# Kernel tuning notes

Hardware: AMD Instinct MI355X
Metric: run time of the kernel (lower is better)

Reference implementation:

```python
import jax, jax.numpy as jnp
import numpy as np

EMBED_DIM = 1024
NUM_HEADS = 16
HEAD_DIM = EMBED_DIM // NUM_HEADS


def setup_inputs() -> dict:
    key = jax.random.key(0)
    ks = jax.random.split(key, 9)
    B, S, D = 2, 2048, EMBED_DIM
    scale = 1.0 / np.sqrt(D)
    x = jax.random.normal(ks[0], (B, S, D), dtype=jnp.float32)
    # Linear params (torch nn.Linear: y = x @ W.T + b); store W as [out, in]
    Wq = jax.random.normal(ks[1], (D, D), dtype=jnp.float32) * scale
    bq = jnp.zeros((D,), dtype=jnp.float32)
    Wk = jax.random.normal(ks[2], (D, D), dtype=jnp.float32) * scale
    bk = jnp.zeros((D,), dtype=jnp.float32)
    Wv = jax.random.normal(ks[3], (D, D), dtype=jnp.float32) * scale
    bv = jnp.zeros((D,), dtype=jnp.float32)
    Wo = jax.random.normal(ks[4], (D, D), dtype=jnp.float32) * scale
    bo = jnp.zeros((D,), dtype=jnp.float32)
    return {"x": x, "Wq": Wq, "bq": bq, "Wk": Wk, "bk": bk,
            "Wv": Wv, "bv": bv, "Wo": Wo, "bo": bo}


def reference(x, Wq, bq, Wk, bk, Wv, bv, Wo, bo):
    B, S, D = x.shape
    H, Hd = NUM_HEADS, HEAD_DIM
    scaling = Hd ** -0.5
    # projections (torch Linear: x @ W.T + b)
    q = (x @ Wq.T + bq).reshape(B, S, H, Hd).transpose(0, 2, 1, 3)  # [B,H,S,Hd]
    k = (x @ Wk.T + bk).reshape(B, S, H, Hd).transpose(0, 2, 1, 3)
    v = (x @ Wv.T + bv).reshape(B, S, H, Hd).transpose(0, 2, 1, 3)
    # full score matrix, as in the original (no flash tiling)
    scores = jnp.einsum('bhqd,bhkd->bhqk', q, k) * scaling  # [B,H,S,S]
    attn = jax.nn.softmax(scores, axis=-1)
    # dropout is identity in eval mode
    out = jnp.einsum('bhqk,bhkd->bhqd', attn, v)  # [B,H,S,Hd]
    out = out.transpose(0, 2, 1, 3).reshape(B, S, D)
    return out @ Wo.T + bo
```

## Files before the change

### kernel.cpp

```cpp
#include <hip/hip_runtime.h>
#include <stdint.h>

typedef unsigned short u16;
typedef short short8 __attribute__((ext_vector_type(8)));
typedef float f32x4 __attribute__((ext_vector_type(4)));
typedef float f32x16 __attribute__((ext_vector_type(16)));
typedef float f32x2 __attribute__((ext_vector_type(2)));

__device__ __forceinline__ u16 f2bf_fast(float f) {
  union { float f; uint32_t u; } x;
  x.f = f;
  return (u16)((x.u + 0x8000u) >> 16);
}

__device__ __forceinline__ uint32_t pack2bf(float lo, float hi) {
  union { float f; uint32_t u; } a, b;
  a.f = lo; b.f = hi;
  return __builtin_amdgcn_perm(b.u + 0x8000u, a.u + 0x8000u, 0x07060302u);
}

__device__ __forceinline__ float bf2f(uint32_t u) {
  union { uint32_t u; float f; } x;
  x.u = u << 16;
  return x.f;
}

__device__ __forceinline__ uint32_t cvtpk(float lo, float hi) {
  uint32_t r;
  asm("v_cvt_pk_bf16_f32 %0, %1, %2" : "=v"(r) : "v"(lo), "v"(hi));
  return r;
}

__device__ __forceinline__ void permswap(uint32_t& a, uint32_t& b) {
  asm("v_permlane32_swap_b32 %0, %1" : "+v"(a), "+v"(b));
}

__device__ __forceinline__ void gload_lds16(const void* g, void* l) {
  __builtin_amdgcn_global_load_lds(
      (const __attribute__((address_space(1))) void*)g,
      (__attribute__((address_space(3))) void*)l, 16, 0, 0);
}

__device__ __forceinline__ f32x4 mfma16(short8 a, short8 b, f32x4 c) {
  return __builtin_amdgcn_mfma_f32_16x16x32_bf16(a, b, c, 0, 0, 0);
}

__device__ __forceinline__ f32x16 mfma32(short8 a, short8 b, f32x16 c) {
  return __builtin_amdgcn_mfma_f32_32x32x16_bf16(a, b, c, 0, 0, 0);
}

#define QSCALE 0.18033688011112042f

__global__ void pack_all(const float* __restrict__ x, const float* __restrict__ wq,
                         const float* __restrict__ wk, const float* __restrict__ wv,
                         const float* __restrict__ wo, u16* __restrict__ xp,
                         u16* __restrict__ wp) {
  const int gi = blockIdx.x * 256 + threadIdx.x;
  const int lane = gi & 63;
  const int kc = (gi >> 6) & 31;
  const int rt = gi >> 11;
  const int col = kc * 32 + (lane >> 4) * 8;
  const float* src;
  int row;
  if (rt < 256) {
    src = x;
    row = rt * 16 + (lane & 15);
  } else {
    const int wti = rt - 256;
    const int widx = wti >> 6;
    src = (widx == 0) ? wq : (widx == 1) ? wk : (widx == 2) ? wv : wo;
    row = (wti & 63) * 16 + (lane & 15);
  }
  const float4* p = (const float4*)(src + (size_t)row * 1024 + col);
  const float4 v0 = p[0], v1 = p[1];
  uint4 o;
  o.x = pack2bf(v0.x, v0.y);
  o.y = pack2bf(v0.z, v0.w);
  o.z = pack2bf(v1.x, v1.y);
  o.w = pack2bf(v1.z, v1.w);
  u16* dst = (rt < 256) ? xp : wp;
  const int og = (rt < 256) ? gi : gi - 524288;
  ((uint4*)dst)[og] = o;
}

__global__ __launch_bounds__(256, 3) void proj_qkv(
    const u16* __restrict__ xp, const u16* __restrict__ wp,
    const float* __restrict__ bq, const float* __restrict__ bk,
    const float* __restrict__ bv, u16* __restrict__ qw, u16* __restrict__ kw,
    u16* __restrict__ vw) {
  __shared__ __align__(16) u16 As[8192];
  __shared__ __align__(16) u16 Bs[8192];
  const int tid = threadIdx.x, lane = tid & 63, w = tid >> 6;
  const int quad = lane >> 4, l15 = lane & 15;

  const int bid = blockIdx.x;
  const int work = (bid & 7) * 96 + (bid >> 3);
  const bool isQK = work < 512;
  int at0, bt0, bm2, bn2;
  const u16 *Ap, *Bp;
  if (isQK) {
    bm2 = work >> 4; bn2 = work & 15;
    Ap = xp; at0 = bm2 * 8;
    Bp = wp; bt0 = bn2 * 8;
  } else {
    const int h = work - 512;
    bm2 = h >> 5; bn2 = h & 31;
    Ap = wp; at0 = 128 + bm2 * 8;
    Bp = xp; bt0 = bn2 * 8;
  }
  const int wr = w >> 1, wc = w & 1;
  const int bm = bm2 * 2 + wr, bn = bn2 * 2 + wc;

  auto stage = [&](int kc, int buf) {
#pragma unroll
    for (int i = 0; i < 4; ++i) {
      const int g = w * 4 + i;
      const int t = g & 7;
      const u16* src = (g < 8)
          ? (Ap + (((at0 + t) << 5) + kc) * 512 + lane * 8)
          : (Bp + (((bt0 + t) << 5) + kc) * 512 + lane * 8);
      u16* dst = ((g < 8) ? As : Bs) + (buf * 8 + t) * 512 + lane * 8;
      gload_lds16(src, dst);
    }
  };

  f32x4 acc[4][4] = {};

  stage(0, 0);
  __syncthreads();

  for (int kc = 0; kc < 32; ++kc) {
    const int cur = kc & 1;
    if (kc < 31) stage(kc + 1, cur ^ 1);

    const u16* Ab = As + cur * 4096;
    const u16* Bb = Bs + cur * 4096;
    short8 af[4], bf[4];
#pragma unroll
    for (int mt = 0; mt < 4; ++mt)
      af[mt] = *(const short8*)&Ab[((wr * 4 + mt) * 64 + lane) * 8];
#pragma unroll
    for (int nt = 0; nt < 4; ++nt)
      bf[nt] = *(const short8*)&Bb[((wc * 4 + nt) * 64 + lane) * 8];

#pragma unroll
    for (int mt = 0; mt < 4; ++mt)
#pragma unroll
      for (int nt = 0; nt < 4; ++nt)
        acc[mt][nt] = mfma16(af[mt], bf[nt], acc[mt][nt]);
    __syncthreads();
  }

#pragma unroll
  for (int nt = 0; nt < 4; ++nt) {
    const int n = bn * 64 + nt * 16 + l15;
#pragma unroll
    for (int mt = 0; mt < 4; ++mt)
#pragma unroll
      for (int r = 0; r < 4; ++r) {
        const int m = bm * 64 + mt * 16 + quad * 4 + r;
        const float a = acc[mt][nt][r];
        if (isQK) {
          const bool isQ = (bn < 16);
          const int nn = isQ ? n : n - 1024;
          const float v = isQ ? (a + bq[nn]) * QSCALE : a + bk[nn];
          u16* op = isQ ? qw : kw;
          const int b = m >> 11, s = m & 2047, hh = nn >> 6, d = nn & 63;
          op[((size_t)((b * 16 + hh) * 2048 + s)) * 64 + d] = f2bf_fast(v);
        } else {
          const float v = a + bv[m];
          const int b = n >> 11, s = n & 2047;
          vw[((size_t)(b * 1024 + m)) * 2048 + s] = f2bf_fast(v);
        }
      }
  }
}

__global__ __launch_bounds__(256, 4) void attn_kernel(
    const u16* __restrict__ Q, const u16* __restrict__ Kt,
    const u16* __restrict__ Vt, u16* __restrict__ awp) {
  __shared__ __align__(16) u16 Sm[16384];
  const int tid = threadIdx.x, lane = tid & 63, w = tid >> 6;
  const int l31 = lane & 31, hi = lane >> 5, l7 = lane & 7;
  const int qt = blockIdx.x;
  const int bh = blockIdx.y;

  const char* Qb = (const char*)(Q + ((size_t)bh * 2048 + qt * 128) * 64);
  const char* Kb = (const char*)(Kt + (size_t)bh * 2048 * 64);
  const char* Vb = (const char*)(Vt + (size_t)bh * 64 * 2048);

  auto stageKV = [&](int kt, int b) {
    u16* Kl = Sm + b * 4096;
    u16* Vl = Sm + 8192 + b * 4096;
#pragma unroll
    for (int i = 0; i < 2; ++i) {
      const int G = (w * 2 + i) * 64 + lane;
      const int r = G >> 3, sl = G & 7;
      gload_lds16(Kb + (size_t)(kt * 64 + r) * 128 + ((sl ^ (r & 7)) * 16),
                  &Kl[G * 8]);
      gload_lds16(Vb + (size_t)r * 4096 + kt * 128 + ((sl ^ (r & 7)) * 16),
                  &Vl[G * 8]);
    }
  };

#pragma unroll
  for (int i = 0; i < 4; ++i) {
    const int G = (w * 4 + i) * 64 + lane;
    const int row = G >> 3, sl = G & 7;
    u16* qdst = (G < 512) ? (Sm + 4096) : (Sm + 12288);
    gload_lds16(Qb + (size_t)row * 128 + ((sl ^ (row & 7)) * 16),
                &qdst[(G & 511) * 8]);
  }
  stageKV(0, 0);
  __syncthreads();

  const u16* qreg = (w < 2) ? (Sm + 4096) : (Sm + 12288);
  const int qr0 = (w & 1) * 32;
  short8 aq[4];
#pragma unroll
  for (int ds = 0; ds < 4; ++ds)
    aq[ds] = *(const short8*)&qreg[(qr0 + l31) * 64 + (((ds << 1) + hi) ^ l7) * 8];
  __syncthreads();

  f32x16 ot[2] = {};
  f32x2 l2 = {0.f, 0.f};

  for (int kt = 0; kt < 32; ++kt) {
    const int buf = kt & 1;
    if (kt < 31) stageKV(kt + 1, buf ^ 1);
    const u16* Kl = Sm + buf * 4096;
    const u16* Vl = Sm + 8192 + buf * 4096;

#pragma unroll
    for (int t = 0; t < 2; ++t) {
      f32x16 st = {};
      __builtin_amdgcn_s_setprio(1);
#pragma unroll
      for (int ds = 0; ds < 4; ++ds) {
        short8 kf = *(const short8*)&Kl[(t * 32 + l31) * 64 +
                                        (((ds << 1) + hi) ^ l7) * 8];
        st = mfma32(kf, aq[ds], st);
      }
      __builtin_amdgcn_s_setprio(0);
      float e[16];
#pragma unroll
      for (int i = 0; i < 16; ++i) e[i] = __builtin_amdgcn_exp2f(st[i]);
#pragma unroll
      for (int i = 0; i < 8; ++i) l2 += (f32x2){e[2 * i], e[2 * i + 1]};

      uint32_t p01 = cvtpk(e[0], e[1]),   p23 = cvtpk(e[2], e[3]);
      uint32_t p45 = cvtpk(e[4], e[5]),   p67 = cvtpk(e[6], e[7]);
      uint32_t p89 = cvtpk(e[8], e[9]),   pAB = cvtpk(e[10], e[11]);
      uint32_t pCD = cvtpk(e[12], e[13]), pEF = cvtpk(e[14], e[15]);
      permswap(p01, p45);
      permswap(p23, p67);
      permswap(p89, pCD);
      permswap(pAB, pEF);
      union { uint32_t u[4]; short8 s; } b0, b1;
      b0.u[0] = p01; b0.u[1] = p23; b0.u[2] = p45; b0.u[3] = p67;
      b1.u[0] = p89; b1.u[1] = pAB; b1.u[2] = pCD; b1.u[3] = pEF;

      __builtin_amdgcn_s_setprio(1);
#pragma unroll
      for (int dt = 0; dt < 2; ++dt) {
#pragma unroll
        for (int s2 = 0; s2 < 2; ++s2) {
          short8 vf = *(const short8*)&Vl[(dt * 32 + l31) * 64 +
                                          ((((t * 2 + s2) << 1) + hi) ^ l7) * 8];
          ot[dt] = mfma32(vf, s2 ? b1.s : b0.s, ot[dt]);
        }
      }
      __builtin_amdgcn_s_setprio(0);
    }
    if (kt < 31) __syncthreads();
  }

  const int b = bh >> 4, h = bh & 15;
  float l = l2.x + l2.y;
  l += __shfl_xor(l, 32);
  const float inv = __builtin_amdgcn_rcpf(l);
  const int rt = b * 128 + qt * 8 + w * 2 + (l31 >> 4);
#pragma unroll
  for (int dt = 0; dt < 2; ++dt) {
    const int kc = h * 2 + dt;
#pragma unroll
    for (int g = 0; g < 4; ++g) {
      const int ln = (lane & 15) + 16 * g;
      uint2 ov;
      ov.x = cvtpk(ot[dt][4 * g + 0] * inv, ot[dt][4 * g + 1] * inv);
      ov.y = cvtpk(ot[dt][4 * g + 2] * inv, ot[dt][4 * g + 3] * inv);
      *(uint2*)(awp + ((size_t)((rt * 32 + kc) * 64 + ln)) * 8 + hi * 4) = ov;
    }
  }
}

__global__ __launch_bounds__(512, 2) void out_proj(const u16* __restrict__ awp,
                                                   const u16* __restrict__ wp,
                                                   const float* __restrict__ bo,
                                                   float* __restrict__ out) {
  __shared__ __align__(16) u16 As[8192];
  __shared__ __align__(16) u16 Bs[8192];
  const int tid = threadIdx.x, lane = tid & 63, w = tid >> 6;
  const int quad = lane >> 4, l15 = lane & 15;

  const int bid = blockIdx.x;
  const int work = (bid & 7) * 32 + (bid >> 3);
  const int bm2 = work >> 3, bn2 = work & 7;
  const int at0 = bm2 * 8, bt0 = 192 + bn2 * 8;
  const int wr = w >> 2, wc = w & 3;

  auto stage = [&](int kc, int buf) {
#pragma unroll
    for (int i = 0; i < 2; ++i) {
      const int g = w * 2 + i;
      const int t = g & 7;
      const u16* src = (g < 8)
          ? (awp + (((at0 + t) << 5) + kc) * 512 + lane * 8)
          : (wp + (((bt0 + t) << 5) + kc) * 512 + lane * 8);
      u16* dst = ((g < 8) ? As : Bs) + (buf * 8 + t) * 512 + lane * 8;
      gload_lds16(src, dst);
    }
  };

  f32x4 acc[4][2] = {};

  stage(0, 0);
  __syncthreads();

  for (int kc = 0; kc < 32; ++kc) {
    const int cur = kc & 1;
    if (kc < 31) stage(kc + 1, cur ^ 1);

    const u16* Ab = As + cur * 4096;
    const u16* Bb = Bs + cur * 4096;
    short8 af[4], bf[2];
#pragma unroll
    for (int mt = 0; mt < 4; ++mt)
      af[mt] = *(const short8*)&Ab[((wr * 4 + mt) * 64 + lane) * 8];
#pragma unroll
    for (int nt = 0; nt < 2; ++nt)
      bf[nt] = *(const short8*)&Bb[((wc * 2 + nt) * 64 + lane) * 8];

#pragma unroll
    for (int mt = 0; mt < 4; ++mt)
#pragma unroll
      for (int nt = 0; nt < 2; ++nt)
        acc[mt][nt] = mfma16(af[mt], bf[nt], acc[mt][nt]);
    __syncthreads();
  }

#pragma unroll
  for (int nt = 0; nt < 2; ++nt) {
    const int n = bn2 * 128 + wc * 32 + nt * 16 + l15;
    const float bb = bo[n];
#pragma unroll
    for (int mt = 0; mt < 4; ++mt)
#pragma unroll
      for (int r = 0; r < 4; ++r) {
        const int m = bm2 * 128 + wr * 64 + mt * 16 + quad * 4 + r;
        out[(size_t)m * 1024 + n] = acc[mt][nt][r] + bb;
      }
  }
}

extern "C" void kernel_launch(void* const* d_in, const int* in_sizes, int n_in,
                              void* d_out, int out_size, void* d_ws, size_t ws_size,
                              hipStream_t stream) {
  const float* x  = (const float*)d_in[0];
  const float* Wq = (const float*)d_in[1];
  const float* bq = (const float*)d_in[2];
  const float* Wk = (const float*)d_in[3];
  const float* bk = (const float*)d_in[4];
  const float* Wv = (const float*)d_in[5];
  const float* bv = (const float*)d_in[6];
  const float* Wo = (const float*)d_in[7];
  const float* bo = (const float*)d_in[8];

  const size_t M4 = (size_t)4 * 1024 * 1024;
  u16* xp  = (u16*)d_ws;
  u16* wp  = xp + M4;
  u16* qw  = wp + M4;
  u16* kw  = qw + M4;
  u16* vw  = kw + M4;
  u16* awp = vw + M4;

  pack_all<<<4096, 256, 0, stream>>>(x, Wq, Wk, Wv, Wo, xp, wp);

  proj_qkv<<<768, 256, 0, stream>>>(xp, wp, bq, bk, bv, qw, kw, vw);

  attn_kernel<<<dim3(16, 32), 256, 0, stream>>>(qw, kw, vw, awp);

  out_proj<<<256, 512, 0, stream>>>(awp, wp, bo, (float*)d_out);
}
```

Measured before the change: 187.6 us.

## Split attention KV sequence across two wave groups with LDS reduction

Doubles attention block size to 512 threads: waves 0-3 and 4-7 each process half of the key/value sequence for the same 128 queries, staging both halves into a larger LDS buffer. Partial outputs and row sums from the second half are reduced through LDS before normalization and store. This halves the serial KV loop length per wave to increase parallelism, but it raises LDS use to 80KB per block, which lowers blocks per CU, and it adds a reduction step with extra barriers.

```diff
diff --git a/kernel.cpp b/kernel.cpp
--- a/kernel.cpp
+++ b/kernel.cpp
@@ -176,12 +176,13 @@
   }
 }
 
-__global__ __launch_bounds__(256, 4) void attn_kernel(
+__global__ __launch_bounds__(512, 4) void attn_kernel(
     const u16* __restrict__ Q, const u16* __restrict__ Kt,
     const u16* __restrict__ Vt, u16* __restrict__ awp) {
-  __shared__ __align__(16) u16 Sm[16384];
+  __shared__ __align__(16) u16 Sm[40960];
   const int tid = threadIdx.x, lane = tid & 63, w = tid >> 6;
   const int l31 = lane & 31, hi = lane >> 5, l7 = lane & 7;
+  const int kh = w >> 2, qg = w & 3;
   const int qt = blockIdx.x;
   const int bh = blockIdx.y;
 
@@ -189,12 +190,13 @@
   const char* Kb = (const char*)(Kt + (size_t)bh * 2048 * 64);
   const char* Vb = (const char*)(Vt + (size_t)bh * 64 * 2048);
 
-  auto stageKV = [&](int kt, int b) {
-    u16* Kl = Sm + b * 4096;
-    u16* Vl = Sm + 8192 + b * 4096;
-#pragma unroll
-    for (int i = 0; i < 2; ++i) {
-      const int G = (w * 2 + i) * 64 + lane;
+  auto stageKV = [&](int j, int buf) {
+#pragma unroll
+    for (int h = 0; h < 2; ++h) {
+      const int kt = h * 16 + j;
+      u16* Kl = Sm + (buf * 2 + h) * 8192;
+      u16* Vl = Kl + 4096;
+      const int G = w * 64 + lane;
       const int r = G >> 3, sl = G & 7;
       gload_lds16(Kb + (size_t)(kt * 64 + r) * 128 + ((sl ^ (r & 7)) * 16),
                   &Kl[G * 8]);
@@ -203,33 +205,29 @@
     }
   };
 
-#pragma unroll
-  for (int i = 0; i < 4; ++i) {
-    const int G = (w * 4 + i) * 64 + lane;
+  u16* Qs = Sm + 32768;
+#pragma unroll
+  for (int i = 0; i < 2; ++i) {
+    const int G = (w * 2 + i) * 64 + lane;
     const int row = G >> 3, sl = G & 7;
-    u16* qdst = (G < 512) ? (Sm + 4096) : (Sm + 12288);
-    gload_lds16(Qb + (size_t)row * 128 + ((sl ^ (row & 7)) * 16),
-                &qdst[(G & 511) * 8]);
+    gload_lds16(Qb + (size_t)row * 128 + ((sl ^ (row & 7)) * 16), &Qs[G * 8]);
   }
   stageKV(0, 0);
   __syncthreads();
 
-  const u16* qreg = (w < 2) ? (Sm + 4096) : (Sm + 12288);
-  const int qr0 = (w & 1) * 32;
   short8 aq[4];
 #pragma unroll
   for (int ds = 0; ds < 4; ++ds)
-    aq[ds] = *(const short8*)&qreg[(qr0 + l31) * 64 + (((ds << 1) + hi) ^ l7) * 8];
-  __syncthreads();
+    aq[ds] = *(const short8*)&Qs[(qg * 32 + l31) * 64 + (((ds << 1) + hi) ^ l7) * 8];
 
   f32x16 ot[2] = {};
   f32x2 l2 = {0.f, 0.f};
 
-  for (int kt = 0; kt < 32; ++kt) {
-    const int buf = kt & 1;
-    if (kt < 31) stageKV(kt + 1, buf ^ 1);
-    const u16* Kl = Sm + buf * 4096;
-    const u16* Vl = Sm + 8192 + buf * 4096;
+  for (int j = 0; j < 16; ++j) {
+    const int buf = j & 1;
+    if (j < 15) stageKV(j + 1, buf ^ 1);
+    const u16* Kl = Sm + (buf * 2 + kh) * 8192;
+    const u16* Vl = Kl + 4096;
 
 #pragma unroll
     for (int t = 0; t < 2; ++t) {
@@ -272,24 +270,46 @@
       }
       __builtin_amdgcn_s_setprio(0);
     }
-    if (kt < 31) __syncthreads();
-  }
-
-  const int b = bh >> 4, h = bh & 15;
+    if (j < 15) __syncthreads();
+  }
+
   float l = l2.x + l2.y;
   l += __shfl_xor(l, 32);
-  const float inv = __builtin_amdgcn_rcpf(l);
-  const int rt = b * 128 + qt * 8 + w * 2 + (l31 >> 4);
-#pragma unroll
-  for (int dt = 0; dt < 2; ++dt) {
-    const int kc = h * 2 + dt;
-#pragma unroll
-    for (int g = 0; g < 4; ++g) {
-      const int ln = (lane & 15) + 16 * g;
-      uint2 ov;
-      ov.x = cvtpk(ot[dt][4 * g + 0] * inv, ot[dt][4 * g + 1] * inv);
-      ov.y = cvtpk(ot[dt][4 * g + 2] * inv, ot[dt][4 * g + 3] * inv);
-      *(uint2*)(awp + ((size_t)((rt * 32 + kc) * 64 + ln)) * 8 + hi * 4) = ov;
+
+  __syncthreads();
+  float* fb = (float*)Sm;
+  if (kh == 1) {
+    float* p = fb + (qg * 64 + lane) * 34;
+#pragma unroll
+    for (int i = 0; i < 8; ++i) {
+      *(f32x2*)(p + 2 * i)      = (f32x2){ot[0][2 * i], ot[0][2 * i + 1]};
+      *(f32x2*)(p + 16 + 2 * i) = (f32x2){ot[1][2 * i], ot[1][2 * i + 1]};
+    }
+    p[32] = l;
+  }
+  __syncthreads();
+  if (kh == 0) {
+    const float* p = fb + (qg * 64 + lane) * 34;
+#pragma unroll
+    for (int i = 0; i < 16; ++i) ot[0][i] += p[i];
+#pragma unroll
+    for (int i = 0; i < 16; ++i) ot[1][i] += p[16 + i];
+    l += p[32];
+    const float inv = __builtin_amdgcn_rcpf(l);
+
+    const int b = bh >> 4, h = bh & 15;
+    const int rt = b * 128 + qt * 8 + qg * 2 + (l31 >> 4);
+#pragma unroll
+    for (int dt = 0; dt < 2; ++dt) {
+      const int kc = h * 2 + dt;
+#pragma unroll
+      for (int g = 0; g < 4; ++g) {
+        const int ln = (lane & 15) + 16 * g;
+        uint2 ov;
+        ov.x = cvtpk(ot[dt][4 * g + 0] * inv, ot[dt][4 * g + 1] * inv);
+        ov.y = cvtpk(ot[dt][4 * g + 2] * inv, ot[dt][4 * g + 3] * inv);
+        *(uint2*)(awp + ((size_t)((rt * 32 + kc) * 64 + ln)) * 8 + hi * 4) = ov;
+      }
     }
   }
 }
@@ -388,7 +408,7 @@
 
   proj_qkv<<<768, 256, 0, stream>>>(xp, wp, bq, bk, bv, qw, kw, vw);
 
-  attn_kernel<<<dim3(16, 32), 256, 0, stream>>>(qw, kw, vw, awp);
+  attn_kernel<<<dim3(16, 32), 512, 0, stream>>>(qw, kw, vw, awp);
 
   out_proj<<<256, 512, 0, stream>>>(awp, wp, bo, (float*)d_out);
 }
```

New measurement: 189.3 us (median of 2 runs). Within noise of the previous version (+0.9%).
